# Kernel tuning notes

Measured on AMD Instinct MI355X. Metric: run time of the kernel, lower is better.

The kernel has to match this reference:

```python
import jax, jax.numpy as jnp
import numpy as np

EMBED_DIM = 1024
NUM_HEADS = 16
HEAD_DIM = EMBED_DIM // NUM_HEADS


def setup_inputs() -> dict:
    key = jax.random.key(0)
    ks = jax.random.split(key, 9)
    B, S, D = 2, 2048, EMBED_DIM
    scale = 1.0 / np.sqrt(D)
    x = jax.random.normal(ks[0], (B, S, D), dtype=jnp.float32)
    mask = jnp.ones((B, S), dtype=jnp.int32)
    # nn.Linear weights: [out_features, in_features]
    Wq = jax.random.normal(ks[1], (D, D), dtype=jnp.float32) * scale
    bq = jnp.zeros((D,), dtype=jnp.float32)
    Wk = jax.random.normal(ks[2], (D, D), dtype=jnp.float32) * scale
    bk = jnp.zeros((D,), dtype=jnp.float32)
    Wv = jax.random.normal(ks[3], (D, D), dtype=jnp.float32) * scale
    bv = jnp.zeros((D,), dtype=jnp.float32)
    Wo = jax.random.normal(ks[4], (D, D), dtype=jnp.float32) * scale
    bo = jnp.zeros((D,), dtype=jnp.float32)
    return {"x": x, "mask": mask, "Wq": Wq, "bq": bq, "Wk": Wk, "bk": bk,
            "Wv": Wv, "bv": bv, "Wo": Wo, "bo": bo}


def reference(x, mask, Wq, bq, Wk, bk, Wv, bv, Wo, bo):
    B, S, D = x.shape
    H, Hd = NUM_HEADS, HEAD_DIM
    q = (x @ Wq.T + bq).reshape(B, S, H, Hd).transpose(0, 2, 1, 3)  # [B,H,S,Hd]
    k = (x @ Wk.T + bk).reshape(B, S, H, Hd).transpose(0, 2, 1, 3)
    v = (x @ Wv.T + bv).reshape(B, S, H, Hd).transpose(0, 2, 1, 3)
    scores = jnp.einsum('bhqd,bhkd->bhqk', q, k) / jnp.sqrt(jnp.float32(Hd))
    m = mask[:, None, None, :]  # [B,1,1,S]
    scores = jnp.where(m == 0, jnp.float32(-1e9), scores)
    attn = jax.nn.softmax(scores, axis=-1)  # dropout p=0 / eval -> identity
    out = jnp.einsum('bhqk,bhkd->bhqd', attn, v)
    out = out.transpose(0, 2, 1, 3).reshape(B, S, D)
    return out @ Wo.T + bo
```

## Files before the change

kernel.cpp:

```cpp
#include <hip/hip_runtime.h>


typedef unsigned short u16;
typedef unsigned int   u32;
typedef __bf16 bf16;
typedef bf16 bf16x8 __attribute__((ext_vector_type(8)));
typedef float f32x4  __attribute__((ext_vector_type(4)));
typedef float f32x16 __attribute__((ext_vector_type(16)));
typedef u16  u16x8  __attribute__((ext_vector_type(8)));
typedef u16  u16x4  __attribute__((ext_vector_type(4)));
typedef u32  u32x4  __attribute__((ext_vector_type(4)));

#define DEV __device__ __forceinline__

#if __has_builtin(__builtin_amdgcn_exp2f)
#define EXP2(x) __builtin_amdgcn_exp2f(x)
#else
#define EXP2(x) exp2f(x)
#endif

DEV void gld_lds16(const void* g, void* l) {
  __builtin_amdgcn_global_load_lds(
      (__attribute__((address_space(1))) void*)(const_cast<void*>(g)),
      (__attribute__((address_space(3))) void*)(l), 16, 0, 0);
}

DEV u16 f2bf(float f) {
  u32 u = __builtin_bit_cast(u32, f);
  u32 lsb = (u >> 16) & 1u;
  u += 0x7fffu + lsb;
  return (u16)(u >> 16);
}

DEV u32 pbf2(float lo, float hi) {
  u32 d;
  asm("v_cvt_pk_bf16_f32 %0, %1, %2" : "=v"(d) : "v"(lo), "v"(hi));
  return d;
}

DEV void pl32swap(u32& a, u32& b) {
  asm("v_permlane32_swap_b32 %0, %1" : "+v"(a), "+v"(b));
}

struct CastArgs {
  const float* src[5];
  u16* dst[5];
  int n4[5];
};

__global__ __launch_bounds__(256) void cast_f32_bf16_kernel(CastArgs a) {
  const int y = blockIdx.y;
  const float4* s = (const float4*)a.src[y];
  u16x4* d = (u16x4*)a.dst[y];
  const int n4 = a.n4[y];
  const int stride = gridDim.x * blockDim.x;
  for (int i = blockIdx.x * blockDim.x + threadIdx.x; i < n4; i += stride) {
    float4 f = s[i];
    u16x4 o;
    o[0] = f2bf(f.x); o[1] = f2bf(f.y); o[2] = f2bf(f.z); o[3] = f2bf(f.w);
    d[i] = o;
  }
}

template<bool OUTF32>
__global__ __launch_bounds__(256, 2) void gemm_nt_kernel(
    const u16* __restrict__ A,
    const u16* __restrict__ B0, const u16* __restrict__ B1, const u16* __restrict__ B2,
    const float* __restrict__ bias0, const float* __restrict__ bias1, const float* __restrict__ bias2,
    void* __restrict__ C0, void* __restrict__ C1, void* __restrict__ C2,
    int M, int N, int K, float alpha0, float alpha1, float alpha2)
{
  __shared__ __attribute__((aligned(16))) u16 As[2][4096];
  __shared__ __attribute__((aligned(16))) u16 Bs[2][4096];

  const int z = blockIdx.z;
  const u16* Bmat   = (z == 0) ? B0 : (z == 1) ? B1 : B2;
  const float* bias = (z == 0) ? bias0 : (z == 1) ? bias1 : bias2;
  void* Cout        = (z == 0) ? C0 : (z == 1) ? C1 : C2;
  const float alpha = (z == 0) ? alpha0 : (z == 1) ? alpha1 : alpha2;

  const int tid  = threadIdx.x;
  const int lane = tid & 63;
  const int w    = tid >> 6;
  const int wr   = w >> 1, wc = w & 1;
  const int l15  = lane & 15, l4 = lane >> 4;
  const int m0   = blockIdx.y * 128;
  const int n0   = blockIdx.x * 128;

  const int u0 = tid;
  const int u1 = tid + 256;
  const int r0 = u0 >> 2, c0s = (u0 & 3) ^ (r0 & 3);
  const int r1 = u1 >> 2, c1s = (u1 & 3) ^ (r1 & 3);
  const size_t K2 = (size_t)K * 2;
  const char* pa0 = (const char*)A + (size_t)(m0 + r0) * K2 + c0s * 16;
  const char* pa1 = (const char*)A + (size_t)(m0 + r1) * K2 + c1s * 16;
  const char* pb0 = (const char*)Bmat + (size_t)(n0 + r0) * K2 + c0s * 16;
  const char* pb1 = (const char*)Bmat + (size_t)(n0 + r1) * K2 + c1s * 16;

  f32x4 acc[4][4] = {};

  const int aoff0 = (wr * 64 + l15) * 64 + ((l4 ^ (l15 & 3)) * 16);
  const int boff0 = (wc * 64 + l15) * 64 + ((l4 ^ (l15 & 3)) * 16);

  gld_lds16(pa0, (char*)As[0] + u0 * 16);
  gld_lds16(pa1, (char*)As[0] + u1 * 16);
  gld_lds16(pb0, (char*)Bs[0] + u0 * 16);
  gld_lds16(pb1, (char*)Bs[0] + u1 * 16);
  __syncthreads();

  int buf = 0;
  for (int k0 = 0; k0 < K; k0 += 32) {
    if (k0 + 32 < K) {
      const size_t ko = (size_t)(k0 + 32) * 2;
      gld_lds16(pa0 + ko, (char*)As[buf ^ 1] + u0 * 16);
      gld_lds16(pa1 + ko, (char*)As[buf ^ 1] + u1 * 16);
      gld_lds16(pb0 + ko, (char*)Bs[buf ^ 1] + u0 * 16);
      gld_lds16(pb1 + ko, (char*)Bs[buf ^ 1] + u1 * 16);
    }
    bf16x8 af[4], bfr[4];
#pragma unroll
    for (int mt = 0; mt < 4; ++mt)
      af[mt] = *(const bf16x8*)((const char*)As[buf] + aoff0 + mt * 16 * 64);
#pragma unroll
    for (int nt = 0; nt < 4; ++nt)
      bfr[nt] = *(const bf16x8*)((const char*)Bs[buf] + boff0 + nt * 16 * 64);
#pragma unroll
    for (int mt = 0; mt < 4; ++mt)
#pragma unroll
      for (int nt = 0; nt < 4; ++nt)
        acc[mt][nt] = __builtin_amdgcn_mfma_f32_16x16x32_bf16(af[mt], bfr[nt], acc[mt][nt], 0, 0, 0);
    __syncthreads();
    buf ^= 1;
  }

  if (!OUTF32 && z == 2) {
#pragma unroll
    for (int nt = 0; nt < 4; ++nt) {
      const int col = n0 + wc * 64 + nt * 16 + l15;
      const float bv = bias[col];
#pragma unroll
      for (int mt = 0; mt < 4; ++mt) {
        const int row0 = m0 + wr * 64 + mt * 16 + l4 * 4;
        const int b = row0 >> 11, s0 = row0 & 2047;
        u16x4 o;
#pragma unroll
        for (int r = 0; r < 4; ++r) o[r] = f2bf(acc[mt][nt][r] + bv);
        *(u16x4*)((u16*)Cout + (size_t)b * 2097152 + (size_t)col * 2048 + s0) = o;
      }
    }
  } else {
#pragma unroll
    for (int nt = 0; nt < 4; ++nt) {
      const int col = n0 + wc * 64 + nt * 16 + l15;
      const float bv = bias[col];
#pragma unroll
      for (int mt = 0; mt < 4; ++mt) {
        const int row = m0 + wr * 64 + mt * 16 + l4 * 4;
#pragma unroll
        for (int r = 0; r < 4; ++r) {
          float v = (acc[mt][nt][r] + bv) * alpha;
          if (OUTF32) ((float*)Cout)[(size_t)(row + r) * N + col] = v;
          else        ((u16*)Cout)[(size_t)(row + r) * N + col] = f2bf(v);
        }
      }
    }
  }
}

__global__ __launch_bounds__(256, 2) void attn_fwd_kernel(
    const u16* __restrict__ Qg, const u16* __restrict__ Kg, const u16* __restrict__ Vtg,
    const int* __restrict__ maskg, u16* __restrict__ Og)
{
  __shared__ __attribute__((aligned(16))) u16 lds[16384];
  __shared__ u32 tzb[4];

  const int tid  = threadIdx.x;
  const int lane = tid & 63;
  const int w    = tid >> 6;
  const int l31  = lane & 31, half = lane >> 5;
  const int qt   = blockIdx.x;
  const int bh   = blockIdx.y;
  const int b    = bh >> 4, h = bh & 15;
  const int qbase = qt * 128 + w * 32;

  {
    const int4* mp = (const int4*)(maskg + b * 2048 + tid * 8);
    const int4 a = mp[0], c = mp[1];
    const bool az = (a.x == 0) | (a.y == 0) | (a.z == 0) | (a.w == 0) |
                    (c.x == 0) | (c.y == 0) | (c.z == 0) | (c.w == 0);
    const unsigned long long bal = __ballot(az);
    if (lane == 0) {
      u32 bits = 0;
#pragma unroll
      for (int t = 0; t < 8; ++t)
        if ((bal >> (8 * t)) & 0xFFull) bits |= (1u << t);
      tzb[w] = bits;
    }
  }

  const int u0 = tid, u1 = tid + 256;
  const int r0 = u0 >> 3, c0 = (u0 & 7) ^ (r0 & 7);
  const int r1 = u1 >> 3, c1 = (u1 & 7) ^ (r1 & 7);
  const char* kp0 = (const char*)Kg + ((size_t)(b * 2048 + r0) * 1024 + h * 64 + c0 * 8) * 2;
  const char* kp1 = (const char*)Kg + ((size_t)(b * 2048 + r1) * 1024 + h * 64 + c1 * 8) * 2;
  const char* vp0 = (const char*)Vtg + ((size_t)b * 2097152 + (size_t)h * 131072 + (size_t)r0 * 2048 + c0 * 8) * 2;
  const char* vp1 = (const char*)Vtg + ((size_t)b * 2097152 + (size_t)h * 131072 + (size_t)r1 * 2048 + c1 * 8) * 2;

  bf16x8 qf[4];
  {
    const char* qrow = (const char*)Qg + ((size_t)(b * 2048 + qbase + l31) * 1024 + h * 64) * 2;
#pragma unroll
    for (int c = 0; c < 4; ++c)
      qf[c] = *(const bf16x8*)(qrow + c * 32 + half * 16);
  }

  const int* mrow_ptr = maskg + b * 2048;

  gld_lds16(kp0, (char*)lds + u0 * 16);
  gld_lds16(kp1, (char*)lds + u1 * 16);
  gld_lds16(vp0, (char*)(lds + 8192) + u0 * 16);
  gld_lds16(vp1, (char*)(lds + 8192) + u1 * 16);
  __syncthreads();

  const u32 tilezero = tzb[0] | (tzb[1] << 8) | (tzb[2] << 16) | (tzb[3] << 24);

  f32x16 oT[2] = {};
  float lpart = 0.f;

  int buf = 0;
  for (int kt = 0; kt < 32; ++kt) {
    if (kt < 31) {
      const size_t ko = (size_t)(kt + 1) * 131072;
      const size_t vo = (size_t)(kt + 1) * 128;
      gld_lds16(kp0 + ko, (char*)(lds + (buf ^ 1) * 4096) + u0 * 16);
      gld_lds16(kp1 + ko, (char*)(lds + (buf ^ 1) * 4096) + u1 * 16);
      gld_lds16(vp0 + vo, (char*)(lds + 8192 + (buf ^ 1) * 4096) + u0 * 16);
      gld_lds16(vp1 + vo, (char*)(lds + 8192 + (buf ^ 1) * 4096) + u1 * 16);
    }

    const char* ktile = (const char*)(lds + buf * 4096);
    const char* vtile = (const char*)(lds + 8192 + buf * 4096);

#pragma unroll
    for (int sub = 0; sub < 2; ++sub) {
      f32x16 st = {};
      const int krow = sub * 32 + l31;
      const char* kbase = ktile + krow * 128;
#pragma unroll
      for (int c = 0; c < 4; ++c) {
        bf16x8 kf = *(const bf16x8*)(kbase + (((c * 2 + half) ^ (krow & 7)) * 16));
        st = __builtin_amdgcn_mfma_f32_32x32x16_bf16(kf, qf[c], st, 0, 0, 0);
      }

      if (tilezero & (1u << kt)) {
        const int kvb = kt * 64 + sub * 32 + half * 4;
#pragma unroll
        for (int r = 0; r < 16; ++r)
          if (mrow_ptr[kvb + (r & 3) + 8 * (r >> 2)] == 0) st[r] = -1e9f;
      }

#pragma unroll
      for (int r = 0; r < 16; ++r) {
        st[r] = EXP2(st[r] - 8.0f);
        lpart += st[r];
      }

      u32 a0 = pbf2(st[0], st[1]),   b0 = pbf2(st[4], st[5]);
      u32 a1 = pbf2(st[2], st[3]),   b1 = pbf2(st[6], st[7]);
      u32 a2 = pbf2(st[8], st[9]),   b2 = pbf2(st[12], st[13]);
      u32 a3 = pbf2(st[10], st[11]), b3 = pbf2(st[14], st[15]);
      pl32swap(a0, b0); pl32swap(a1, b1); pl32swap(a2, b2); pl32swap(a3, b3);
      u32x4 wlo = {a0, a1, b0, b1}, whi = {a2, a3, b2, b3};
      bf16x8 Blo = __builtin_bit_cast(bf16x8, wlo);
      bf16x8 Bhi = __builtin_bit_cast(bf16x8, whi);

#pragma unroll
      for (int hdt = 0; hdt < 2; ++hdt) {
        const int vrow = hdt * 32 + l31;
        const char* vbase = vtile + vrow * 128;
        bf16x8 vlo = *(const bf16x8*)(vbase + (((sub * 4 + half) ^ (vrow & 7)) * 16));
        bf16x8 vhi = *(const bf16x8*)(vbase + (((sub * 4 + 2 + half) ^ (vrow & 7)) * 16));
        oT[hdt] = __builtin_amdgcn_mfma_f32_32x32x16_bf16(vlo, Blo, oT[hdt], 0, 0, 0);
        oT[hdt] = __builtin_amdgcn_mfma_f32_32x32x16_bf16(vhi, Bhi, oT[hdt], 0, 0, 0);
      }
    }

    __syncthreads();
    buf ^= 1;
  }

  const float ltot = lpart + __shfl_xor(lpart, 32);
  const float inv = 1.0f / ltot;

  u16* sc = lds + w * 2304;
#pragma unroll
  for (int hdt = 0; hdt < 2; ++hdt)
#pragma unroll
    for (int run = 0; run < 4; ++run) {
      u16x4 o4;
#pragma unroll
      for (int i = 0; i < 4; ++i) o4[i] = f2bf(oT[hdt][run * 4 + i] * inv);
      const int hd0 = hdt * 32 + run * 8 + half * 4;
      *(u16x4*)(sc + l31 * 72 + hd0) = o4;
    }
#pragma unroll
  for (int rep = 0; rep < 4; ++rep) {
    const int q = rep * 8 + (lane >> 3);
    u16x8 v = *(const u16x8*)(sc + q * 72 + (lane & 7) * 8);
    const size_t tok = (size_t)(b * 2048 + qbase + q);
    *(u16x8*)(Og + tok * 1024 + h * 64 + (lane & 7) * 8) = v;
  }
}

extern "C" void kernel_launch(void* const* d_in, const int* in_sizes, int n_in,
                              void* d_out, int out_size, void* d_ws, size_t ws_size,
                              hipStream_t stream) {
  const float* x  = (const float*)d_in[0];
  const int* mask = (const int*)d_in[1];
  const float* Wq = (const float*)d_in[2];
  const float* bq = (const float*)d_in[3];
  const float* Wk = (const float*)d_in[4];
  const float* bk = (const float*)d_in[5];
  const float* Wv = (const float*)d_in[6];
  const float* bv = (const float*)d_in[7];
  const float* Wo = (const float*)d_in[8];
  const float* bo = (const float*)d_in[9];
  float* out = (float*)d_out;

  const int Mtok = 2 * 2048;
  const int D = 1024;

  const size_t need = (size_t)Mtok * D * 2 * 5 + (size_t)D * D * 2 * 4;
  if (ws_size < need) return;

  char* p = (char*)d_ws;
  u16* xb  = (u16*)p; p += (size_t)Mtok * D * 2;
  u16* wqb = (u16*)p; p += (size_t)D * D * 2;
  u16* wkb = (u16*)p; p += (size_t)D * D * 2;
  u16* wvb = (u16*)p; p += (size_t)D * D * 2;
  u16* wob = (u16*)p; p += (size_t)D * D * 2;
  u16* Qb  = (u16*)p; p += (size_t)Mtok * D * 2;
  u16* Kb  = (u16*)p; p += (size_t)Mtok * D * 2;
  u16* Vtb = (u16*)p; p += (size_t)Mtok * D * 2;
  u16* Ob  = (u16*)p; p += (size_t)Mtok * D * 2;

  CastArgs ca;
  ca.src[0] = x;  ca.dst[0] = xb;  ca.n4[0] = Mtok * D / 4;
  ca.src[1] = Wq; ca.dst[1] = wqb; ca.n4[1] = D * D / 4;
  ca.src[2] = Wk; ca.dst[2] = wkb; ca.n4[2] = D * D / 4;
  ca.src[3] = Wv; ca.dst[3] = wvb; ca.n4[3] = D * D / 4;
  ca.src[4] = Wo; ca.dst[4] = wob; ca.n4[4] = D * D / 4;
  cast_f32_bf16_kernel<<<dim3(256, 5), 256, 0, stream>>>(ca);

  const float qalpha = 0.125f * 1.44269504088896340736f;
  gemm_nt_kernel<false><<<dim3(D / 128, Mtok / 128, 3), 256, 0, stream>>>(
      xb, wqb, wkb, wvb, bq, bk, bv, Qb, Kb, Vtb, Mtok, D, D, qalpha, 1.0f, 1.0f);

  attn_fwd_kernel<<<dim3(2048 / 128, 32), 256, 0, stream>>>(Qb, Kb, Vtb, mask, Ob);

  gemm_nt_kernel<true><<<dim3(D / 128, Mtok / 128, 1), 256, 0, stream>>>(
      Ob, wob, wob, wob, bo, bo, bo, out, out, out, Mtok, D, D, 1.0f, 1.0f, 1.0f);
}
```

Measured before the change: 120.9 us.

## Split key tile across wave pairs, share K fragments across two query groups

```diff
diff --git a/kernel.cpp b/kernel.cpp
--- a/kernel.cpp
+++ b/kernel.cpp
@@ -40,6 +40,17 @@
 
 DEV void pl32swap(u32& a, u32& b) {
   asm("v_permlane32_swap_b32 %0, %1" : "+v"(a), "+v"(b));
+}
+
+DEV void pack_pt(const f32x16& st, bf16x8& Blo, bf16x8& Bhi) {
+  u32 a0 = pbf2(st[0], st[1]),   b0 = pbf2(st[4], st[5]);
+  u32 a1 = pbf2(st[2], st[3]),   b1 = pbf2(st[6], st[7]);
+  u32 a2 = pbf2(st[8], st[9]),   b2 = pbf2(st[12], st[13]);
+  u32 a3 = pbf2(st[10], st[11]), b3 = pbf2(st[14], st[15]);
+  pl32swap(a0, b0); pl32swap(a1, b1); pl32swap(a2, b2); pl32swap(a3, b3);
+  u32x4 wlo = {a0, a1, b0, b1}, whi = {a2, a3, b2, b3};
+  Blo = __builtin_bit_cast(bf16x8, wlo);
+  Bhi = __builtin_bit_cast(bf16x8, whi);
 }
 
 struct CastArgs {
@@ -171,7 +182,7 @@
     const u16* __restrict__ Qg, const u16* __restrict__ Kg, const u16* __restrict__ Vtg,
     const int* __restrict__ maskg, u16* __restrict__ Og)
 {
-  __shared__ __attribute__((aligned(16))) u16 lds[16384];
+  __shared__ __attribute__((aligned(16))) u16 lds[18432];
   __shared__ u32 tzb[4];
 
   const int tid  = threadIdx.x;
@@ -181,7 +192,9 @@
   const int qt   = blockIdx.x;
   const int bh   = blockIdx.y;
   const int b    = bh >> 4, h = bh & 15;
-  const int qbase = qt * 128 + w * 32;
+  const int p    = w >> 1;
+  const int sub  = w & 1;
+  const int qbase = qt * 128 + p * 64;
 
   {
     const int4* mp = (const int4*)(maskg + b * 2048 + tid * 8);
@@ -206,109 +219,164 @@
   const char* vp0 = (const char*)Vtg + ((size_t)b * 2097152 + (size_t)h * 131072 + (size_t)r0 * 2048 + c0 * 8) * 2;
   const char* vp1 = (const char*)Vtg + ((size_t)b * 2097152 + (size_t)h * 131072 + (size_t)r1 * 2048 + c1 * 8) * 2;
 
-  bf16x8 qf[4];
+  bf16x8 qf[2][4];
   {
-    const char* qrow = (const char*)Qg + ((size_t)(b * 2048 + qbase + l31) * 1024 + h * 64) * 2;
-#pragma unroll
-    for (int c = 0; c < 4; ++c)
-      qf[c] = *(const bf16x8*)(qrow + c * 32 + half * 16);
-  }
+    const char* qrow0 = (const char*)Qg + ((size_t)(b * 2048 + qbase + l31) * 1024 + h * 64) * 2;
+    const char* qrow1 = (const char*)Qg + ((size_t)(b * 2048 + qbase + 32 + l31) * 1024 + h * 64) * 2;
+#pragma unroll
+    for (int c = 0; c < 4; ++c) {
+      qf[0][c] = *(const bf16x8*)(qrow0 + c * 32 + half * 16);
+      qf[1][c] = *(const bf16x8*)(qrow1 + c * 32 + half * 16);
+    }
+  }
+
+  bf16x8 ones;
+#pragma unroll
+  for (int i = 0; i < 8; ++i) ones[i] = (bf16)1.0f;
 
   const int* mrow_ptr = maskg + b * 2048;
 
   gld_lds16(kp0, (char*)lds + u0 * 16);
   gld_lds16(kp1, (char*)lds + u1 * 16);
-  gld_lds16(vp0, (char*)(lds + 8192) + u0 * 16);
-  gld_lds16(vp1, (char*)(lds + 8192) + u1 * 16);
+  gld_lds16(vp0, (char*)lds + 16384 + u0 * 16);
+  gld_lds16(vp1, (char*)lds + 16384 + u1 * 16);
   __syncthreads();
 
   const u32 tilezero = tzb[0] | (tzb[1] << 8) | (tzb[2] << 16) | (tzb[3] << 24);
 
-  f32x16 oT[2] = {};
-  float lpart = 0.f;
+  f32x16 oT00 = {}, oT01 = {}, oT10 = {}, oT11 = {};
+  f32x16 lacc0 = {}, lacc1 = {};
 
   int buf = 0;
   for (int kt = 0; kt < 32; ++kt) {
     if (kt < 31) {
       const size_t ko = (size_t)(kt + 1) * 131072;
       const size_t vo = (size_t)(kt + 1) * 128;
-      gld_lds16(kp0 + ko, (char*)(lds + (buf ^ 1) * 4096) + u0 * 16);
-      gld_lds16(kp1 + ko, (char*)(lds + (buf ^ 1) * 4096) + u1 * 16);
-      gld_lds16(vp0 + vo, (char*)(lds + 8192 + (buf ^ 1) * 4096) + u0 * 16);
-      gld_lds16(vp1 + vo, (char*)(lds + 8192 + (buf ^ 1) * 4096) + u1 * 16);
-    }
-
-    const char* ktile = (const char*)(lds + buf * 4096);
-    const char* vtile = (const char*)(lds + 8192 + buf * 4096);
-
-#pragma unroll
-    for (int sub = 0; sub < 2; ++sub) {
-      f32x16 st = {};
-      const int krow = sub * 32 + l31;
-      const char* kbase = ktile + krow * 128;
-#pragma unroll
-      for (int c = 0; c < 4; ++c) {
-        bf16x8 kf = *(const bf16x8*)(kbase + (((c * 2 + half) ^ (krow & 7)) * 16));
-        st = __builtin_amdgcn_mfma_f32_32x32x16_bf16(kf, qf[c], st, 0, 0, 0);
-      }
-
-      if (tilezero & (1u << kt)) {
-        const int kvb = kt * 64 + sub * 32 + half * 4;
-#pragma unroll
-        for (int r = 0; r < 16; ++r)
-          if (mrow_ptr[kvb + (r & 3) + 8 * (r >> 2)] == 0) st[r] = -1e9f;
-      }
-
-#pragma unroll
-      for (int r = 0; r < 16; ++r) {
-        st[r] = EXP2(st[r] - 8.0f);
-        lpart += st[r];
-      }
-
-      u32 a0 = pbf2(st[0], st[1]),   b0 = pbf2(st[4], st[5]);
-      u32 a1 = pbf2(st[2], st[3]),   b1 = pbf2(st[6], st[7]);
-      u32 a2 = pbf2(st[8], st[9]),   b2 = pbf2(st[12], st[13]);
-      u32 a3 = pbf2(st[10], st[11]), b3 = pbf2(st[14], st[15]);
-      pl32swap(a0, b0); pl32swap(a1, b1); pl32swap(a2, b2); pl32swap(a3, b3);
-      u32x4 wlo = {a0, a1, b0, b1}, whi = {a2, a3, b2, b3};
-      bf16x8 Blo = __builtin_bit_cast(bf16x8, wlo);
-      bf16x8 Bhi = __builtin_bit_cast(bf16x8, whi);
-
-#pragma unroll
-      for (int hdt = 0; hdt < 2; ++hdt) {
-        const int vrow = hdt * 32 + l31;
-        const char* vbase = vtile + vrow * 128;
-        bf16x8 vlo = *(const bf16x8*)(vbase + (((sub * 4 + half) ^ (vrow & 7)) * 16));
-        bf16x8 vhi = *(const bf16x8*)(vbase + (((sub * 4 + 2 + half) ^ (vrow & 7)) * 16));
-        oT[hdt] = __builtin_amdgcn_mfma_f32_32x32x16_bf16(vlo, Blo, oT[hdt], 0, 0, 0);
-        oT[hdt] = __builtin_amdgcn_mfma_f32_32x32x16_bf16(vhi, Bhi, oT[hdt], 0, 0, 0);
-      }
+      gld_lds16(kp0 + ko, (char*)lds + (buf ^ 1) * 8192 + u0 * 16);
+      gld_lds16(kp1 + ko, (char*)lds + (buf ^ 1) * 8192 + u1 * 16);
+      gld_lds16(vp0 + vo, (char*)lds + 16384 + (buf ^ 1) * 8192 + u0 * 16);
+      gld_lds16(vp1 + vo, (char*)lds + 16384 + (buf ^ 1) * 8192 + u1 * 16);
+    }
+
+    f32x16 st0 = {}, st1 = {};
+    const int krow = sub * 32 + l31;
+    const char* kbase = (const char*)lds + buf * 8192 + krow * 128;
+#pragma unroll
+    for (int c = 0; c < 4; ++c) {
+      bf16x8 kf = *(const bf16x8*)(kbase + (((c * 2 + half) ^ (krow & 7)) * 16));
+      st0 = __builtin_amdgcn_mfma_f32_32x32x16_bf16(kf, qf[0][c], st0, 0, 0, 0);
+      st1 = __builtin_amdgcn_mfma_f32_32x32x16_bf16(kf, qf[1][c], st1, 0, 0, 0);
+    }
+
+    if (tilezero & (1u << kt)) {
+      const int kvb = kt * 64 + sub * 32 + half * 4;
+#pragma unroll
+      for (int r = 0; r < 16; ++r)
+        if (mrow_ptr[kvb + (r & 3) + 8 * (r >> 2)] == 0) { st0[r] = -1e9f; st1[r] = -1e9f; }
+    }
+
+#pragma unroll
+    for (int r = 0; r < 16; ++r) {
+      st0[r] = EXP2(st0[r] - 8.0f);
+      st1[r] = EXP2(st1[r] - 8.0f);
+    }
+
+    bf16x8 Blo0, Bhi0, Blo1, Bhi1;
+    pack_pt(st0, Blo0, Bhi0);
+    pack_pt(st1, Blo1, Bhi1);
+
+    lacc0 = __builtin_amdgcn_mfma_f32_32x32x16_bf16(ones, Blo0, lacc0, 0, 0, 0);
+    lacc0 = __builtin_amdgcn_mfma_f32_32x32x16_bf16(ones, Bhi0, lacc0, 0, 0, 0);
+    lacc1 = __builtin_amdgcn_mfma_f32_32x32x16_bf16(ones, Blo1, lacc1, 0, 0, 0);
+    lacc1 = __builtin_amdgcn_mfma_f32_32x32x16_bf16(ones, Bhi1, lacc1, 0, 0, 0);
+
+    {
+      const int vrow0 = l31;
+      const char* vb0 = (const char*)lds + 16384 + buf * 8192 + vrow0 * 128;
+      bf16x8 vlo = *(const bf16x8*)(vb0 + (((sub * 4 + half) ^ (vrow0 & 7)) * 16));
+      bf16x8 vhi = *(const bf16x8*)(vb0 + (((sub * 4 + 2 + half) ^ (vrow0 & 7)) * 16));
+      oT00 = __builtin_amdgcn_mfma_f32_32x32x16_bf16(vlo, Blo0, oT00, 0, 0, 0);
+      oT00 = __builtin_amdgcn_mfma_f32_32x32x16_bf16(vhi, Bhi0, oT00, 0, 0, 0);
+      oT01 = __builtin_amdgcn_mfma_f32_32x32x16_bf16(vlo, Blo1, oT01, 0, 0, 0);
+      oT01 = __builtin_amdgcn_mfma_f32_32x32x16_bf16(vhi, Bhi1, oT01, 0, 0, 0);
+    }
+    {
+      const int vrow1 = 32 + l31;
+      const char* vb1 = (const char*)lds + 16384 + buf * 8192 + vrow1 * 128;
+      bf16x8 vlo = *(const bf16x8*)(vb1 + (((sub * 4 + half) ^ (vrow1 & 7)) * 16));
+      bf16x8 vhi = *(const bf16x8*)(vb1 + (((sub * 4 + 2 + half) ^ (vrow1 & 7)) * 16));
+      oT10 = __builtin_amdgcn_mfma_f32_32x32x16_bf16(vlo, Blo0, oT10, 0, 0, 0);
+      oT10 = __builtin_amdgcn_mfma_f32_32x32x16_bf16(vhi, Bhi0, oT10, 0, 0, 0);
+      oT11 = __builtin_amdgcn_mfma_f32_32x32x16_bf16(vlo, Blo1, oT11, 0, 0, 0);
+      oT11 = __builtin_amdgcn_mfma_f32_32x32x16_bf16(vhi, Bhi1, oT11, 0, 0, 0);
     }
 
     __syncthreads();
     buf ^= 1;
   }
 
-  const float ltot = lpart + __shfl_xor(lpart, 32);
-  const float inv = 1.0f / ltot;
-
-  u16* sc = lds + w * 2304;
-#pragma unroll
-  for (int hdt = 0; hdt < 2; ++hdt)
-#pragma unroll
-    for (int run = 0; run < 4; ++run) {
-      u16x4 o4;
-#pragma unroll
-      for (int i = 0; i < 4; ++i) o4[i] = f2bf(oT[hdt][run * 4 + i] * inv);
-      const int hd0 = hdt * 32 + run * 8 + half * 4;
-      *(u16x4*)(sc + l31 * 72 + hd0) = o4;
-    }
-#pragma unroll
-  for (int rep = 0; rep < 4; ++rep) {
-    const int q = rep * 8 + (lane >> 3);
-    u16x8 v = *(const u16x8*)(sc + q * 72 + (lane & 7) * 8);
-    const size_t tok = (size_t)(b * 2048 + qbase + q);
-    *(u16x8*)(Og + tok * 1024 + h * 64 + (lane & 7) * 8) = v;
+  float* Ll = (float*)((char*)lds + 32768);
+  if (sub == 1) {
+    if (lane < 32) {
+      Ll[p * 64 + l31]      = lacc0[0];
+      Ll[p * 64 + 32 + l31] = lacc1[0];
+    }
+    float* R1w = (float*)((char*)lds + p * 16384);
+#define WR(OT, HDT, QG)                                            \
+    _Pragma("unroll") for (int r = 0; r < 16; ++r) {               \
+      const int row = HDT * 32 + (r & 3) + 8 * (r >> 2) + 4 * half;\
+      R1w[row * 64 + QG * 32 + l31] = OT[r];                       \
+    }
+    WR(oT00, 0, 0) WR(oT01, 0, 1) WR(oT10, 1, 0) WR(oT11, 1, 1)
+#undef WR
+  }
+  __syncthreads();
+
+  u16x4 ov[2][2][4];
+  if (sub == 0) {
+    const float* R1 = (const float*)((char*)lds + p * 16384);
+    const float linv0 = 1.0f / (lacc0[0] + Ll[p * 64 + l31]);
+    const float linv1 = 1.0f / (lacc1[0] + Ll[p * 64 + 32 + l31]);
+#define RD(OT, HDT, QG, LINV)                                            \
+    _Pragma("unroll") for (int run = 0; run < 4; ++run) {                \
+      u16x4 o4;                                                          \
+      _Pragma("unroll") for (int i = 0; i < 4; ++i) {                    \
+        const int row = HDT * 32 + i + 8 * run + 4 * half;               \
+        o4[i] = f2bf((OT[run * 4 + i] + R1[row * 64 + QG * 32 + l31]) * LINV); \
+      }                                                                  \
+      ov[HDT][QG][run] = o4;                                             \
+    }
+    RD(oT00, 0, 0, linv0) RD(oT01, 0, 1, linv1)
+    RD(oT10, 1, 0, linv0) RD(oT11, 1, 1, linv1)
+#undef RD
+  }
+  __syncthreads();
+
+  if (sub == 0) {
+    char* sc = (char*)lds + p * 9216;
+#pragma unroll
+    for (int hdt = 0; hdt < 2; ++hdt)
+#pragma unroll
+      for (int qg = 0; qg < 2; ++qg)
+#pragma unroll
+        for (int run = 0; run < 4; ++run) {
+          const int hd0 = hdt * 32 + run * 8 + half * 4;
+          *(u16x4*)(sc + (qg * 32 + l31) * 144 + hd0 * 2) = ov[hdt][qg][run];
+        }
+  }
+  __syncthreads();
+
+  {
+    const int q  = tid >> 1;
+    const int ph = q >> 6, ql = q & 63;
+    const char* sc = (const char*)lds + ph * 9216;
+    const size_t rowoff = (size_t)(b * 2048 + qt * 128 + q) * 1024 + h * 64;
+#pragma unroll
+    for (int u = 0; u < 4; ++u) {
+      const int ch = (tid & 1) * 4 + u;
+      u16x8 v = *(const u16x8*)(sc + ql * 144 + ch * 16);
+      *(u16x8*)(Og + rowoff + ch * 8) = v;
+    }
   }
 }
 
```

Result: slower. 124.9 us (+3.3%).

## Use 128x64 tiles for output GEMM and MFMA-based softmax row sums

Applied to the files above, without the earlier changes.

```diff
diff --git a/kernel.cpp b/kernel.cpp
--- a/kernel.cpp
+++ b/kernel.cpp
@@ -62,16 +62,17 @@
   }
 }
 
-template<bool OUTF32>
-__global__ __launch_bounds__(256, 2) void gemm_nt_kernel(
+template<bool OUTF32, int BN>
+__global__ __launch_bounds__(256, 3) void gemm_nt_kernel(
     const u16* __restrict__ A,
     const u16* __restrict__ B0, const u16* __restrict__ B1, const u16* __restrict__ B2,
     const float* __restrict__ bias0, const float* __restrict__ bias1, const float* __restrict__ bias2,
     void* __restrict__ C0, void* __restrict__ C1, void* __restrict__ C2,
     int M, int N, int K, float alpha0, float alpha1, float alpha2)
 {
+  constexpr int MT = (BN == 128) ? 4 : 2;
   __shared__ __attribute__((aligned(16))) u16 As[2][4096];
-  __shared__ __attribute__((aligned(16))) u16 Bs[2][4096];
+  __shared__ __attribute__((aligned(16))) u16 Bs[2][BN * 32];
 
   const int z = blockIdx.z;
   const u16* Bmat   = (z == 0) ? B0 : (z == 1) ? B1 : B2;
@@ -82,10 +83,12 @@
   const int tid  = threadIdx.x;
   const int lane = tid & 63;
   const int w    = tid >> 6;
-  const int wr   = w >> 1, wc = w & 1;
   const int l15  = lane & 15, l4 = lane >> 4;
   const int m0   = blockIdx.y * 128;
-  const int n0   = blockIdx.x * 128;
+  const int n0   = blockIdx.x * BN;
+
+  const int rowbase = (BN == 128) ? (w >> 1) * 64 : w * 32;
+  const int colbase = (BN == 128) ? (w & 1) * 64 : 0;
 
   const int u0 = tid;
   const int u1 = tid + 256;
@@ -97,15 +100,15 @@
   const char* pb0 = (const char*)Bmat + (size_t)(n0 + r0) * K2 + c0s * 16;
   const char* pb1 = (const char*)Bmat + (size_t)(n0 + r1) * K2 + c1s * 16;
 
-  f32x4 acc[4][4] = {};
-
-  const int aoff0 = (wr * 64 + l15) * 64 + ((l4 ^ (l15 & 3)) * 16);
-  const int boff0 = (wc * 64 + l15) * 64 + ((l4 ^ (l15 & 3)) * 16);
+  f32x4 acc[MT][4] = {};
+
+  const int aoff0 = (rowbase + l15) * 64 + ((l4 ^ (l15 & 3)) * 16);
+  const int boff0 = (colbase + l15) * 64 + ((l4 ^ (l15 & 3)) * 16);
 
   gld_lds16(pa0, (char*)As[0] + u0 * 16);
   gld_lds16(pa1, (char*)As[0] + u1 * 16);
   gld_lds16(pb0, (char*)Bs[0] + u0 * 16);
-  gld_lds16(pb1, (char*)Bs[0] + u1 * 16);
+  if (BN == 128) gld_lds16(pb1, (char*)Bs[0] + u1 * 16);
   __syncthreads();
 
   int buf = 0;
@@ -115,17 +118,17 @@
       gld_lds16(pa0 + ko, (char*)As[buf ^ 1] + u0 * 16);
       gld_lds16(pa1 + ko, (char*)As[buf ^ 1] + u1 * 16);
       gld_lds16(pb0 + ko, (char*)Bs[buf ^ 1] + u0 * 16);
-      gld_lds16(pb1 + ko, (char*)Bs[buf ^ 1] + u1 * 16);
-    }
-    bf16x8 af[4], bfr[4];
-#pragma unroll
-    for (int mt = 0; mt < 4; ++mt)
+      if (BN == 128) gld_lds16(pb1 + ko, (char*)Bs[buf ^ 1] + u1 * 16);
+    }
+    bf16x8 af[MT], bfr[4];
+#pragma unroll
+    for (int mt = 0; mt < MT; ++mt)
       af[mt] = *(const bf16x8*)((const char*)As[buf] + aoff0 + mt * 16 * 64);
 #pragma unroll
     for (int nt = 0; nt < 4; ++nt)
       bfr[nt] = *(const bf16x8*)((const char*)Bs[buf] + boff0 + nt * 16 * 64);
 #pragma unroll
-    for (int mt = 0; mt < 4; ++mt)
+    for (int mt = 0; mt < MT; ++mt)
 #pragma unroll
       for (int nt = 0; nt < 4; ++nt)
         acc[mt][nt] = __builtin_amdgcn_mfma_f32_16x16x32_bf16(af[mt], bfr[nt], acc[mt][nt], 0, 0, 0);
@@ -136,11 +139,11 @@
   if (!OUTF32 && z == 2) {
 #pragma unroll
     for (int nt = 0; nt < 4; ++nt) {
-      const int col = n0 + wc * 64 + nt * 16 + l15;
+      const int col = n0 + colbase + nt * 16 + l15;
       const float bv = bias[col];
 #pragma unroll
-      for (int mt = 0; mt < 4; ++mt) {
-        const int row0 = m0 + wr * 64 + mt * 16 + l4 * 4;
+      for (int mt = 0; mt < MT; ++mt) {
+        const int row0 = m0 + rowbase + mt * 16 + l4 * 4;
         const int b = row0 >> 11, s0 = row0 & 2047;
         u16x4 o;
 #pragma unroll
@@ -151,11 +154,11 @@
   } else {
 #pragma unroll
     for (int nt = 0; nt < 4; ++nt) {
-      const int col = n0 + wc * 64 + nt * 16 + l15;
+      const int col = n0 + colbase + nt * 16 + l15;
       const float bv = bias[col];
 #pragma unroll
-      for (int mt = 0; mt < 4; ++mt) {
-        const int row = m0 + wr * 64 + mt * 16 + l4 * 4;
+      for (int mt = 0; mt < MT; ++mt) {
+        const int row = m0 + rowbase + mt * 16 + l4 * 4;
 #pragma unroll
         for (int r = 0; r < 4; ++r) {
           float v = (acc[mt][nt][r] + bv) * alpha;
@@ -171,7 +174,7 @@
     const u16* __restrict__ Qg, const u16* __restrict__ Kg, const u16* __restrict__ Vtg,
     const int* __restrict__ maskg, u16* __restrict__ Og)
 {
-  __shared__ __attribute__((aligned(16))) u16 lds[16384];
+  __shared__ __attribute__((aligned(16))) u16 lds[17408];
   __shared__ u32 tzb[4];
 
   const int tid  = threadIdx.x;
@@ -214,6 +217,10 @@
       qf[c] = *(const bf16x8*)(qrow + c * 32 + half * 16);
   }
 
+  bf16x8 ones;
+#pragma unroll
+  for (int i = 0; i < 8; ++i) ones[i] = (bf16)1.0f;
+
   const int* mrow_ptr = maskg + b * 2048;
 
   gld_lds16(kp0, (char*)lds + u0 * 16);
@@ -225,7 +232,7 @@
   const u32 tilezero = tzb[0] | (tzb[1] << 8) | (tzb[2] << 16) | (tzb[3] << 24);
 
   f32x16 oT[2] = {};
-  float lpart = 0.f;
+  f32x16 lacc = {};
 
   int buf = 0;
   for (int kt = 0; kt < 32; ++kt) {
@@ -260,10 +267,8 @@
       }
 
 #pragma unroll
-      for (int r = 0; r < 16; ++r) {
+      for (int r = 0; r < 16; ++r)
         st[r] = EXP2(st[r] - 8.0f);
-        lpart += st[r];
-      }
 
       u32 a0 = pbf2(st[0], st[1]),   b0 = pbf2(st[4], st[5]);
       u32 a1 = pbf2(st[2], st[3]),   b1 = pbf2(st[6], st[7]);
@@ -274,6 +279,9 @@
       bf16x8 Blo = __builtin_bit_cast(bf16x8, wlo);
       bf16x8 Bhi = __builtin_bit_cast(bf16x8, whi);
 
+      lacc = __builtin_amdgcn_mfma_f32_32x32x16_bf16(ones, Blo, lacc, 0, 0, 0);
+      lacc = __builtin_amdgcn_mfma_f32_32x32x16_bf16(ones, Bhi, lacc, 0, 0, 0);
+
 #pragma unroll
       for (int hdt = 0; hdt < 2; ++hdt) {
         const int vrow = hdt * 32 + l31;
@@ -289,9 +297,7 @@
     buf ^= 1;
   }
 
-  const float ltot = lpart + __shfl_xor(lpart, 32);
-  const float inv = 1.0f / ltot;
-
+  const float inv = 1.0f / lacc[0];
   u16* sc = lds + w * 2304;
 #pragma unroll
   for (int hdt = 0; hdt < 2; ++hdt)
@@ -303,6 +309,7 @@
       const int hd0 = hdt * 32 + run * 8 + half * 4;
       *(u16x4*)(sc + l31 * 72 + hd0) = o4;
     }
+  __syncthreads();
 #pragma unroll
   for (int rep = 0; rep < 4; ++rep) {
     const int q = rep * 8 + (lane >> 3);
@@ -353,11 +360,11 @@
   cast_f32_bf16_kernel<<<dim3(256, 5), 256, 0, stream>>>(ca);
 
   const float qalpha = 0.125f * 1.44269504088896340736f;
-  gemm_nt_kernel<false><<<dim3(D / 128, Mtok / 128, 3), 256, 0, stream>>>(
+  gemm_nt_kernel<false, 128><<<dim3(D / 128, Mtok / 128, 3), 256, 0, stream>>>(
       xb, wqb, wkb, wvb, bq, bk, bv, Qb, Kb, Vtb, Mtok, D, D, qalpha, 1.0f, 1.0f);
 
   attn_fwd_kernel<<<dim3(2048 / 128, 32), 256, 0, stream>>>(Qb, Kb, Vtb, mask, Ob);
 
-  gemm_nt_kernel<true><<<dim3(D / 128, Mtok / 128, 1), 256, 0, stream>>>(
+  gemm_nt_kernel<true, 64><<<dim3(D / 64, Mtok / 128, 1), 256, 0, stream>>>(
       Ob, wob, wob, wob, bo, bo, bo, out, out, out, Mtok, D, D, 1.0f, 1.0f, 1.0f);
 }
```

Result: faster. 117.8 us, median of 3 (-2.6%).
